# Optimization experiments

Hardware: AMD Instinct MI355X
Metric: run time of the kernel (lower is better)

## Reference

```python
import jax, jax.numpy as jnp
import numpy as np

N = 50000   # nodes
E = 400000  # edges
R = 35      # num_relations
B = 12      # num_bases
C = 128     # hidden_conv_dim (heads=1)
T = 4       # node types: load, gen, load_gen, ext
HL = 38     # hidden_lin_dim
OUT = 2


def setup_inputs() -> dict:
    key = jax.random.key(0)
    ks = jax.random.split(key, 24)
    s = 0.1  # param scale
    inp = {
        'x': jax.random.normal(ks[0], (N, 2), jnp.float32),
        'edge_index': jax.random.randint(ks[1], (2, E), 0, N, jnp.int32),
        'edge_type': jax.random.randint(ks[2], (E,), 0, R, jnp.int32),
        'edge_attr': jax.random.normal(ks[3], (E, 2), jnp.float32),
        'node_type': jax.random.randint(ks[4], (N,), 0, T, jnp.int32),
        'basis': jax.random.normal(ks[5], (B, 2, C), jnp.float32) * s,
        'att_rel': jax.random.normal(ks[6], (R, B), jnp.float32) * s,
        'q_att': jax.random.normal(ks[7], (C, 1), jnp.float32) * s,
        'k_att': jax.random.normal(ks[8], (C, 1), jnp.float32) * s,
        'e_att': jax.random.normal(ks[9], (C, 1), jnp.float32) * s,
        'lin_edge_W': jax.random.normal(ks[10], (2, C), jnp.float32) * s,
        'conv_bias': jax.random.normal(ks[11], (C,), jnp.float32) * s,
        'lin0_W': jax.random.normal(ks[12], (T, C, HL), jnp.float32) * s,
        'lin0_b': jax.random.normal(ks[13], (T, HL), jnp.float32) * s,
        'lin1_W': jax.random.normal(ks[14], (T, HL, HL), jnp.float32) * s,
        'lin1_b': jax.random.normal(ks[15], (T, HL), jnp.float32) * s,
        'lin2_W': jax.random.normal(ks[16], (T, HL, HL), jnp.float32) * s,
        'lin2_b': jax.random.normal(ks[17], (T, HL), jnp.float32) * s,
        'fin_W': jax.random.normal(ks[18], (T, HL, OUT), jnp.float32) * s,
        'fin_b': jax.random.normal(ks[19], (T, OUT), jnp.float32) * s,
    }
    return inp


def _segment_softmax(alpha, dst, n):
    # PyG softmax: max is detached, eps=1e-16 on the denominator
    amax = jax.lax.stop_gradient(jax.ops.segment_max(alpha, dst, num_segments=n))
    ex = jnp.exp(alpha - amax[dst])
    den = jax.ops.segment_sum(ex, dst, num_segments=n) + 1e-16
    return ex / den[dst]


def _per_type_linear(xv, W, b, t):
    # apply node-type-specific Linear: [N,d] x [T,d,h] -> pick row type
    y = jnp.einsum('nd,tdh->nth', xv, W)              # [N,T,h]
    y = jnp.take_along_axis(y, t[:, None, None], axis=1)[:, 0]
    return y + b[t]


def reference(x, edge_index, edge_type, edge_attr, node_type,
              basis, att_rel, q_att, k_att, e_att, lin_edge_W, conv_bias,
              lin0_W, lin0_b, lin1_W, lin1_b, lin2_W, lin2_b, fin_W, fin_b):
    n = x.shape[0]
    src, dst = edge_index[0], edge_index[1]
    # RGATConv with basis decomposition: per-relation weight [R, in=2, C]
    w = jnp.einsum('rb,bio->rio', att_rel, basis)
    w_e = w[edge_type]                                 # [E,2,C] edge gather
    out_i = jnp.einsum('ei,eic->ec', x[dst], w_e)      # [E,C]
    out_j = jnp.einsum('ei,eic->ec', x[src], w_e)      # [E,C]
    ke = (edge_attr @ lin_edge_W) @ e_att              # [E,1]
    alpha = out_i @ q_att + out_j @ k_att + ke         # additive self-attention
    alpha = jax.nn.leaky_relu(alpha, 0.2)
    alpha = _segment_softmax(alpha, dst, n)            # across-relation segment softmax
    msg = alpha * out_j                                # heads=1 -> [E,C]
    agg = jax.ops.segment_sum(msg, dst, num_segments=n) + conv_bias
    h = jax.nn.leaky_relu(agg, 0.2)                    # forward activation (dropout: eval)
    t = node_type
    h = _per_type_linear(jax.nn.relu(h), lin0_W, lin0_b, t)
    h = _per_type_linear(jax.nn.relu(h), lin1_W, lin1_b, t)
    h = _per_type_linear(jax.nn.relu(h), lin2_W, lin2_b, t)
    out = _per_type_linear(h, fin_W, fin_b, t)         # [N,2]
    # load nodes (type 0): second output passes through abs
    load_out = jnp.concatenate([out[:, :1], jnp.abs(out[:, 1:2])], axis=1)
    return jnp.where((t == 0)[:, None], load_out, out)
```

## Files before the change

### kernel.cpp

```cpp
#include <hip/hip_runtime.h>
#include <math.h>

#define N_NODES 50000
#define N_EDGES 400000
#define R_REL   35
#define B_BASES 12
#define C_DIM   128
#define HL_DIM  38
#define RI2     70
#define NP      50304
#define NB_HIST 196
#define NBUCK   786
#define EPB     2048
#define CAP     704

#define OFF_WT     0
#define OFF_WQ     8960
#define OFF_WK     9030
#define OFF_LE     9100
#define OFF_META   9104
#define OFF_HBLK   9120
#define OFF_PERM   10688
#define OFF_INV    60688
#define OFF_ECUR   110992
#define OFF_EREC   111780

#define ST    0
#define WT    4760
#define HH    0
#define Y0T   0
#define Y1T   3264
#define Y2T   0
#define W1S   8192
#define W2S   9720
#define W0F   13720
#define SM_DINV 18888
#define SM_FW   18952
#define SM_FB   19028
#define LDS_FLOATS 19030

__global__ __launch_bounds__(256) void k_init(const int* __restrict__ node_type,
                                              const float* __restrict__ basis,
                                              const float* __restrict__ att_rel,
                                              const float* __restrict__ q_att,
                                              const float* __restrict__ k_att,
                                              const float* __restrict__ e_att,
                                              const float* __restrict__ lin_edge_W,
                                              float* __restrict__ ws) {
    int b = blockIdx.x, tid = threadIdx.x;
    if (b < NB_HIST) {
        __shared__ int lh[4];
        if (tid < 4) lh[tid] = 0;
        __syncthreads();
        int i = b * 256 + tid;
        if (i < N_NODES) atomicAdd(&lh[node_type[i]], 1);
        __syncthreads();
        if (tid < 4) ((int*)(ws + OFF_HBLK))[b * 4 + tid] = lh[tid];
    } else if (b < NB_HIST + 35) {
        int idx = (b - NB_HIST) * 256 + tid;
        if (idx < RI2 * C_DIM) {
            int c  = idx & (C_DIM - 1);
            int ri = idx >> 7;
            int r = ri >> 1, ii = ri & 1;
            float acc = 0.f;
            #pragma unroll
            for (int bb = 0; bb < B_BASES; ++bb)
                acc += att_rel[r * B_BASES + bb] * basis[(bb * 2 + ii) * C_DIM + c];
            ws[OFF_WT + idx] = acc;
        }
    } else if (b == NB_HIST + 35) {
        for (int i = tid; i < NBUCK; i += 256) ((int*)(ws + OFF_ECUR))[i] = 0;
    } else {
        int lane = tid & 63, wv = tid >> 6;
        int u = (b - (NB_HIST + 36)) * 4 + wv;
        if (u < 2 * RI2) {
            int ri = (u < RI2) ? u : (u - RI2);
            int r = ri >> 1, ii = ri & 1;
            const float* av = att_rel + r * B_BASES;
            const float* bs = basis + ii * C_DIM;
            float w1 = 0.f, w2 = 0.f;
            #pragma unroll
            for (int bb = 0; bb < B_BASES; ++bb) {
                float a = av[bb];
                w1 += a * bs[bb * 2 * C_DIM + lane];
                w2 += a * bs[bb * 2 * C_DIM + 64 + lane];
            }
            const float* qk = (u < RI2) ? q_att : k_att;
            float s = w1 * qk[lane] + w2 * qk[64 + lane];
            #pragma unroll
            for (int off = 32; off; off >>= 1) s += __shfl_xor(s, off, 64);
            if (lane == 0) ws[((u < RI2) ? OFF_WQ : OFF_WK) + ri] = s;
        } else if (u < 2 * RI2 + 2) {
            int j = u - 2 * RI2;
            const float* er = lin_edge_W + j * C_DIM;
            float s = er[lane] * e_att[lane] + er[64 + lane] * e_att[64 + lane];
            #pragma unroll
            for (int off = 32; off; off >>= 1) s += __shfl_xor(s, off, 64);
            if (lane == 0) ws[OFF_LE + j] = s;
        }
    }
}

__global__ __launch_bounds__(256) void k_perm(const int* __restrict__ node_type,
                                              float* __restrict__ ws) {
    __shared__ int lh[NB_HIST * 4];
    __shared__ int pre[4], tot[4], basel[4];
    __shared__ int wcnt[4][4];
    int tid = threadIdx.x;
    int lane = tid & 63, wv = tid >> 6;
    const int* hblk = (const int*)(ws + OFF_HBLK);
    for (int i = tid; i < NB_HIST * 4; i += 256) lh[i] = hblk[i];
    __syncthreads();
    if (tid < 4) {
        int run = 0, mypre = 0;
        for (int bb = 0; bb < NB_HIST; ++bb) {
            if (bb == (int)blockIdx.x) mypre = run;
            run += lh[bb * 4 + tid];
        }
        pre[tid] = mypre;
        tot[tid] = run;
    }
    __syncthreads();
    if (tid == 0) {
        int t0 = tot[0], t1 = tot[1], t2 = tot[2];
        int b1 = ((t0 + 63) >> 6) << 6;
        int b2 = b1 + (((t1 + 63) >> 6) << 6);
        int b3 = b2 + (((t2 + 63) >> 6) << 6);
        basel[0] = 0; basel[1] = b1; basel[2] = b2; basel[3] = b3;
        if (blockIdx.x == 0) {
            int* meta = (int*)(ws + OFF_META);
            meta[0] = t0; meta[1] = t1; meta[2] = t2; meta[3] = tot[3];
            meta[4] = 0;  meta[5] = b1; meta[6] = b2; meta[7] = b3;
        }
    }
    __syncthreads();
    int n = blockIdx.x * 256 + tid;
    bool active = n < N_NODES;
    int ty = active ? node_type[n] : -1;
    int myrank = 0;
    #pragma unroll
    for (int t = 0; t < 4; ++t) {
        unsigned long long m = __ballot(ty == t);
        if (lane == 0) wcnt[wv][t] = __popcll(m);
        if (ty == t) myrank = __popcll(m & ((1ULL << lane) - 1ULL));
    }
    __syncthreads();
    if (active) {
        int prew = 0;
        for (int w2 = 0; w2 < wv; ++w2) prew += wcnt[w2][ty];
        int p = basel[ty] + pre[ty] + prew + myrank;
        ((int*)(ws + OFF_PERM))[n] = p;
        ((int*)(ws + OFF_INV))[p] = n;
    }
}

__global__ __launch_bounds__(256) void k_escatter(const float* __restrict__ x,
                                                  const int* __restrict__ edge_index,
                                                  const int* __restrict__ edge_type,
                                                  const float* __restrict__ edge_attr,
                                                  float* __restrict__ ws) {
    __shared__ int hist[NBUCK];
    __shared__ int sbase[NBUCK];
    __shared__ float swq[RI2], swk[RI2], sle[2];
    int tid = threadIdx.x;
    for (int i = tid; i < NBUCK; i += 256) hist[i] = 0;
    if (tid < RI2) { swq[tid] = ws[OFF_WQ + tid]; swk[tid] = ws[OFF_WK + tid]; }
    if (tid < 2) sle[tid] = ws[OFF_LE + tid];
    __syncthreads();

    const int* perm = (const int*)(ws + OFF_PERM);
    int base = blockIdx.x * EPB;
    int   rb[8], rm[8];
    float rex[8], rsx[8], rsy[8];
    #pragma unroll
    for (int k = 0; k < 8; ++k) {
        int e = base + k * 256 + tid;
        rb[k] = -1;
        if (e < N_EDGES) {
            int src = edge_index[e];
            int dst = edge_index[N_EDGES + e];
            int r   = edge_type[e];
            int p   = perm[dst];
            float2 ea = *(const float2*)(edge_attr + 2 * e);
            float2 xs = *(const float2*)(x + 2 * src);
            float2 xd = *(const float2*)(x + 2 * dst);
            float alpha = xd.x * swq[2 * r] + xd.y * swq[2 * r + 1]
                        + xs.x * swk[2 * r] + xs.y * swk[2 * r + 1]
                        + ea.x * sle[0]     + ea.y * sle[1];
            alpha = alpha > 0.f ? alpha : 0.2f * alpha;
            float ex = __expf(alpha);
            rb[k]  = p >> 6;
            rm[k]  = (r << 6) | (p & 63);
            rex[k] = ex;
            rsx[k] = ex * xs.x;
            rsy[k] = ex * xs.y;
            atomicAdd(&hist[rb[k]], 1);
        }
    }
    __syncthreads();
    int* gcur = (int*)(ws + OFF_ECUR);
    for (int i = tid; i < NBUCK; i += 256) {
        int c = hist[i];
        sbase[i] = (c > 0) ? atomicAdd(&gcur[i], c) : 0;
    }
    __syncthreads();
    float4* rec = (float4*)(ws + OFF_EREC);
    #pragma unroll
    for (int k = 0; k < 8; ++k) {
        if (rb[k] >= 0) {
            int slot = atomicAdd(&sbase[rb[k]], 1);
            rec[(size_t)rb[k] * CAP + slot] =
                make_float4(__int_as_float(rm[k]), rex[k], rsx[k], rsy[k]);
        }
    }
}

__global__ __launch_bounds__(256) void k_node(
        const float* __restrict__ ws, const float* __restrict__ conv_bias,
        const float* __restrict__ lin0_W, const float* __restrict__ lin0_b,
        const float* __restrict__ lin1_W, const float* __restrict__ lin1_b,
        const float* __restrict__ lin2_W, const float* __restrict__ lin2_b,
        const float* __restrict__ fin_W,  const float* __restrict__ fin_b,
        float* __restrict__ out) {
    __shared__ float L[LDS_FLOATS];
    int tid  = threadIdx.x;
    int lane = tid & 63;
    int wv   = tid >> 6;
    int p0   = blockIdx.x * 64;

    const int* meta = (const int*)(ws + OFF_META);
    int b1 = meta[5], b2 = meta[6], b3 = meta[7];
    int t  = (p0 >= b1) + (p0 >= b2) + (p0 >= b3);
    int bp = meta[4 + t];
    int cnt = meta[t];

    for (int i = tid; i < RI2 * 68; i += 256) L[ST + i] = 0.f;
    if (tid < 64) L[SM_DINV + tid] = 0.f;
    if (tid >= 64 && tid < 142) {
        int i = tid - 64;
        if (i < 76) L[SM_FW + i] = fin_W[t * 76 + i];
        else        L[SM_FB + i - 76] = fin_b[t * 2 + i - 76];
    }
    const float* wT_g = ws + OFF_WT;
    for (int i4 = tid; i4 < 2240; i4 += 256) {
        float4 v = ((const float4*)wT_g)[i4];
        *(float4*)&L[WT + i4 * 4] = v;
    }
    const float* W0g = lin0_W + t * C_DIM * HL_DIM;
    for (int i = tid; i < C_DIM * HL_DIM; i += 256) {
        int cc = i / 38, j = i - cc * 38;
        L[W0F + cc * 40 + j] = W0g[i];
    }
    __syncthreads();

    {
        int ecnt = ((const int*)(ws + OFF_ECUR))[blockIdx.x];
        const float4* rec = (const float4*)(ws + OFF_EREC) + (size_t)blockIdx.x * CAP;
        for (int i = tid; i < ecnt; i += 256) {
            float4 v = rec[i];
            int m = __float_as_int(v.x);
            int n = m & 63, r = m >> 6;
            atomicAdd(&L[ST + (2 * r) * 68 + n],     v.z);
            atomicAdd(&L[ST + (2 * r + 1) * 68 + n], v.w);
            atomicAdd(&L[SM_DINV + n],               v.y);
        }
    }
    __syncthreads();
    if (tid < 64) L[SM_DINV + tid] = 1.0f / (L[SM_DINV + tid] + 1e-16f);

    int ng = lane & 15, cg_ = lane >> 4;
    int c0 = wv * 32 + cg_ * 8;
    float acc[32];
    #pragma unroll
    for (int i = 0; i < 32; ++i) acc[i] = 0.f;
    #pragma unroll 5
    for (int kk = 0; kk < RI2; ++kk) {
        float4 a4 = *(const float4*)&L[ST + kk * 68 + ng * 4];
        float4 wa = *(const float4*)&L[WT + kk * 128 + c0];
        float4 wc = *(const float4*)&L[WT + kk * 128 + c0 + 4];
        float a_[4] = {a4.x, a4.y, a4.z, a4.w};
        float w_[8] = {wa.x, wa.y, wa.z, wa.w, wc.x, wc.y, wc.z, wc.w};
        #pragma unroll
        for (int ni = 0; ni < 4; ++ni)
            #pragma unroll
            for (int ci = 0; ci < 8; ++ci)
                acc[ni * 8 + ci] += a_[ni] * w_[ci];
    }
    __syncthreads();

    {
        float4 dv = *(const float4*)&L[SM_DINV + ng * 4];
        float d_[4] = {dv.x, dv.y, dv.z, dv.w};
        #pragma unroll
        for (int ci = 0; ci < 8; ++ci) {
            float cb = conv_bias[c0 + ci];
            float4 hv;
            float h0 = acc[0 * 8 + ci] * d_[0] + cb;
            float h1 = acc[1 * 8 + ci] * d_[1] + cb;
            float h2 = acc[2 * 8 + ci] * d_[2] + cb;
            float h3 = acc[3 * 8 + ci] * d_[3] + cb;
            hv.x = h0 > 0.f ? h0 : 0.f;
            hv.y = h1 > 0.f ? h1 : 0.f;
            hv.z = h2 > 0.f ? h2 : 0.f;
            hv.w = h3 > 0.f ? h3 : 0.f;
            *(float4*)&L[HH + (c0 + ci) * 64 + ng * 4] = hv;
        }
    }
    {
        const float* W1g = lin1_W + t * HL_DIM * HL_DIM;
        const float* W2g = lin2_W + t * HL_DIM * HL_DIM;
        for (int i = tid; i < HL_DIM * HL_DIM; i += 256) {
            int cc = i / 38, j = i - cc * 38;
            L[W1S + cc * 40 + j] = W1g[i];
            L[W2S + cc * 40 + j] = W2g[i];
        }
    }
    __syncthreads();

    int jg = lane >> 4;
    int j0 = wv * 16 + jg * 4;
    float acc2[16];
    #pragma unroll
    for (int i = 0; i < 16; ++i) acc2[i] = 0.f;
    if (wv < 3) {
        #pragma unroll 4
        for (int kk = 0; kk < C_DIM; ++kk) {
            float4 a4 = *(const float4*)&L[HH + kk * 64 + ng * 4];
            float4 w4 = *(const float4*)&L[W0F + kk * 40 + j0];
            float a_[4] = {a4.x, a4.y, a4.z, a4.w};
            float w_[4] = {w4.x, w4.y, w4.z, w4.w};
            #pragma unroll
            for (int ni = 0; ni < 4; ++ni)
                #pragma unroll
                for (int ji = 0; ji < 4; ++ji)
                    acc2[ni * 4 + ji] += a_[ni] * w_[ji];
        }
    }
    __syncthreads();

    if (wv < 3) {
        #pragma unroll
        for (int ji = 0; ji < 4; ++ji) {
            int j = j0 + ji;
            float b = (j < HL_DIM) ? lin0_b[t * HL_DIM + j] : 0.f;
            float4 yv;
            float y0 = acc2[0 * 4 + ji] + b;
            float y1 = acc2[1 * 4 + ji] + b;
            float y2 = acc2[2 * 4 + ji] + b;
            float y3 = acc2[3 * 4 + ji] + b;
            yv.x = y0 > 0.f ? y0 : 0.f;
            yv.y = y1 > 0.f ? y1 : 0.f;
            yv.z = y2 > 0.f ? y2 : 0.f;
            yv.w = y3 > 0.f ? y3 : 0.f;
            *(float4*)&L[Y0T + j * 68 + ng * 4] = yv;
        }
    }
    __syncthreads();

    if (wv < 3) {
        float acc3[16];
        #pragma unroll
        for (int i = 0; i < 16; ++i) acc3[i] = 0.f;
        #pragma unroll 2
        for (int kk = 0; kk < HL_DIM; ++kk) {
            float4 a4 = *(const float4*)&L[Y0T + kk * 68 + ng * 4];
            float4 w4 = *(const float4*)&L[W1S + kk * 40 + j0];
            float a_[4] = {a4.x, a4.y, a4.z, a4.w};
            float w_[4] = {w4.x, w4.y, w4.z, w4.w};
            #pragma unroll
            for (int ni = 0; ni < 4; ++ni)
                #pragma unroll
                for (int ji = 0; ji < 4; ++ji)
                    acc3[ni * 4 + ji] += a_[ni] * w_[ji];
        }
        #pragma unroll
        for (int ji = 0; ji < 4; ++ji) {
            int j = j0 + ji;
            float b = (j < HL_DIM) ? lin1_b[t * HL_DIM + j] : 0.f;
            float4 yv;
            float y0 = acc3[0 * 4 + ji] + b;
            float y1 = acc3[1 * 4 + ji] + b;
            float y2 = acc3[2 * 4 + ji] + b;
            float y3 = acc3[3 * 4 + ji] + b;
            yv.x = y0 > 0.f ? y0 : 0.f;
            yv.y = y1 > 0.f ? y1 : 0.f;
            yv.z = y2 > 0.f ? y2 : 0.f;
            yv.w = y3 > 0.f ? y3 : 0.f;
            *(float4*)&L[Y1T + j * 68 + ng * 4] = yv;
        }
    }
    __syncthreads();

    if (wv < 3) {
        float acc4[16];
        #pragma unroll
        for (int i = 0; i < 16; ++i) acc4[i] = 0.f;
        #pragma unroll 2
        for (int kk = 0; kk < HL_DIM; ++kk) {
            float4 a4 = *(const float4*)&L[Y1T + kk * 68 + ng * 4];
            float4 w4 = *(const float4*)&L[W2S + kk * 40 + j0];
            float a_[4] = {a4.x, a4.y, a4.z, a4.w};
            float w_[4] = {w4.x, w4.y, w4.z, w4.w};
            #pragma unroll
            for (int ni = 0; ni < 4; ++ni)
                #pragma unroll
                for (int ji = 0; ji < 4; ++ji)
                    acc4[ni * 4 + ji] += a_[ni] * w_[ji];
        }
        #pragma unroll
        for (int ji = 0; ji < 4; ++ji) {
            int j = j0 + ji;
            float b = (j < HL_DIM) ? lin2_b[t * HL_DIM + j] : 0.f;
            float4 yv;
            yv.x = acc4[0 * 4 + ji] + b;
            yv.y = acc4[1 * 4 + ji] + b;
            yv.z = acc4[2 * 4 + ji] + b;
            yv.w = acc4[3 * 4 + ji] + b;
            *(float4*)&L[Y2T + j * 68 + ng * 4] = yv;
        }
    }
    __syncthreads();

    if (tid < 64) {
        int p = p0 + tid;
        bool valid = (p - bp) < cnt;
        float o0 = L[SM_FB], o1 = L[SM_FB + 1];
        for (int jj = 0; jj < HL_DIM; ++jj) {
            float v = L[Y2T + jj * 68 + tid];
            float2 f = *(const float2*)&L[SM_FW + jj * 2];
            o0 += v * f.x;
            o1 += v * f.y;
        }
        if (t == 0) o1 = fabsf(o1);
        if (valid) {
            int orig = ((const int*)(ws + OFF_INV))[p];
            ((float2*)out)[orig] = make_float2(o0, o1);
        }
    }
}

extern "C" void kernel_launch(void* const* d_in, const int* in_sizes, int n_in,
                              void* d_out, int out_size, void* d_ws, size_t ws_size,
                              hipStream_t stream) {
    const float* x          = (const float*)d_in[0];
    const int*   edge_index = (const int*)  d_in[1];
    const int*   edge_type  = (const int*)  d_in[2];
    const float* edge_attr  = (const float*)d_in[3];
    const int*   node_type  = (const int*)  d_in[4];
    const float* basis      = (const float*)d_in[5];
    const float* att_rel    = (const float*)d_in[6];
    const float* q_att      = (const float*)d_in[7];
    const float* k_att      = (const float*)d_in[8];
    const float* e_att      = (const float*)d_in[9];
    const float* lin_edge_W = (const float*)d_in[10];
    const float* conv_bias  = (const float*)d_in[11];
    const float* lin0_W     = (const float*)d_in[12];
    const float* lin0_b     = (const float*)d_in[13];
    const float* lin1_W     = (const float*)d_in[14];
    const float* lin1_b     = (const float*)d_in[15];
    const float* lin2_W     = (const float*)d_in[16];
    const float* lin2_b     = (const float*)d_in[17];
    const float* fin_W      = (const float*)d_in[18];
    const float* fin_b      = (const float*)d_in[19];

    float* ws  = (float*)d_ws;
    float* out = (float*)d_out;

    k_init    <<<NB_HIST + 35 + 1 + 36, 256, 0, stream>>>(node_type, basis, att_rel,
                                                          q_att, k_att, e_att, lin_edge_W, ws);
    k_perm    <<<NB_HIST, 256, 0, stream>>>(node_type, ws);
    k_escatter<<<NB_HIST, 256, 0, stream>>>(x, edge_index, edge_type, edge_attr, ws);
    k_node    <<<NBUCK, 256, 0, stream>>>(ws, conv_bias,
                                          lin0_W, lin0_b, lin1_W, lin1_b,
                                          lin2_W, lin2_b, fin_W, fin_b, out);
}
```

Baseline: 172.9 us.

## Read node-MLP weights from padded global buffers instead of staging in LDS

k_init now repacks lin0/lin1/lin2 weights into padded (stride 40) global workspace buffers. k_node stops copying the relation weight table and MLP weights into shared memory and reads them directly from global/L2, which shrinks LDS from ~76KB to ~33KB per block and adds a launch bound of 4 blocks. The aim is to remove per-block staging traffic and raise occupancy, at the cost of broadcast-style global loads inside the inner GEMM loops and possible register pressure from the tighter launch bound.

```diff
diff --git a/kernel.cpp b/kernel.cpp
--- a/kernel.cpp
+++ b/kernel.cpp
@@ -24,20 +24,19 @@
 #define OFF_INV    60688
 #define OFF_ECUR   110992
 #define OFF_EREC   111780
+#define OFF_W0P    2325156
+#define OFF_W1P    2345636
+#define OFF_W2P    2351716
 
 #define ST    0
-#define WT    4760
 #define HH    0
 #define Y0T   0
 #define Y1T   3264
 #define Y2T   0
-#define W1S   8192
-#define W2S   9720
-#define W0F   13720
-#define SM_DINV 18888
-#define SM_FW   18952
-#define SM_FB   19028
-#define LDS_FLOATS 19030
+#define SM_DINV 8192
+#define SM_FW   8256
+#define SM_FB   8332
+#define LDS_FLOATS 8334
 
 __global__ __launch_bounds__(256) void k_init(const int* __restrict__ node_type,
                                               const float* __restrict__ basis,
@@ -46,6 +45,9 @@
                                               const float* __restrict__ k_att,
                                               const float* __restrict__ e_att,
                                               const float* __restrict__ lin_edge_W,
+                                              const float* __restrict__ lin0_W,
+                                              const float* __restrict__ lin1_W,
+                                              const float* __restrict__ lin2_W,
                                               float* __restrict__ ws) {
     int b = blockIdx.x, tid = threadIdx.x;
     if (b < NB_HIST) {
@@ -70,7 +72,7 @@
         }
     } else if (b == NB_HIST + 35) {
         for (int i = tid; i < NBUCK; i += 256) ((int*)(ws + OFF_ECUR))[i] = 0;
-    } else {
+    } else if (b < NB_HIST + 36 + 36) {
         int lane = tid & 63, wv = tid >> 6;
         int u = (b - (NB_HIST + 36)) * 4 + wv;
         if (u < 2 * RI2) {
@@ -97,6 +99,21 @@
             #pragma unroll
             for (int off = 32; off; off >>= 1) s += __shfl_xor(s, off, 64);
             if (lane == 0) ws[OFF_LE + j] = s;
+        }
+    } else {
+        int g = (b - (NB_HIST + 36 + 36)) * 256 + tid;
+        for (int idx = g; idx < 4 * C_DIM * HL_DIM; idx += 16 * 256) {
+            int tt = idx / (C_DIM * HL_DIM);
+            int rem = idx - tt * (C_DIM * HL_DIM);
+            int cc = rem / HL_DIM, j = rem - cc * HL_DIM;
+            ws[OFF_W0P + tt * (C_DIM * 40) + cc * 40 + j] = lin0_W[idx];
+        }
+        for (int idx = g; idx < 4 * HL_DIM * HL_DIM; idx += 16 * 256) {
+            int tt = idx / (HL_DIM * HL_DIM);
+            int rem = idx - tt * (HL_DIM * HL_DIM);
+            int cc = rem / HL_DIM, j = rem - cc * HL_DIM;
+            ws[OFF_W1P + tt * (HL_DIM * 40) + cc * 40 + j] = lin1_W[idx];
+            ws[OFF_W2P + tt * (HL_DIM * 40) + cc * 40 + j] = lin2_W[idx];
         }
     }
 }
@@ -215,13 +232,11 @@
     }
 }
 
-__global__ __launch_bounds__(256) void k_node(
+__global__ __launch_bounds__(256, 4) void k_node(
         const float* __restrict__ ws, const float* __restrict__ conv_bias,
-        const float* __restrict__ lin0_W, const float* __restrict__ lin0_b,
-        const float* __restrict__ lin1_W, const float* __restrict__ lin1_b,
-        const float* __restrict__ lin2_W, const float* __restrict__ lin2_b,
-        const float* __restrict__ fin_W,  const float* __restrict__ fin_b,
-        float* __restrict__ out) {
+        const float* __restrict__ lin0_b, const float* __restrict__ lin1_b,
+        const float* __restrict__ lin2_b, const float* __restrict__ fin_W,
+        const float* __restrict__ fin_b, float* __restrict__ out) {
     __shared__ float L[LDS_FLOATS];
     int tid  = threadIdx.x;
     int lane = tid & 63;
@@ -234,22 +249,13 @@
     int bp = meta[4 + t];
     int cnt = meta[t];
 
-    for (int i = tid; i < RI2 * 68; i += 256) L[ST + i] = 0.f;
+    for (int i4 = tid; i4 < (RI2 * 68) / 4; i4 += 256)
+        *(float4*)&L[ST + i4 * 4] = make_float4(0.f, 0.f, 0.f, 0.f);
     if (tid < 64) L[SM_DINV + tid] = 0.f;
     if (tid >= 64 && tid < 142) {
         int i = tid - 64;
         if (i < 76) L[SM_FW + i] = fin_W[t * 76 + i];
         else        L[SM_FB + i - 76] = fin_b[t * 2 + i - 76];
-    }
-    const float* wT_g = ws + OFF_WT;
-    for (int i4 = tid; i4 < 2240; i4 += 256) {
-        float4 v = ((const float4*)wT_g)[i4];
-        *(float4*)&L[WT + i4 * 4] = v;
-    }
-    const float* W0g = lin0_W + t * C_DIM * HL_DIM;
-    for (int i = tid; i < C_DIM * HL_DIM; i += 256) {
-        int cc = i / 38, j = i - cc * 38;
-        L[W0F + cc * 40 + j] = W0g[i];
     }
     __syncthreads();
 
@@ -270,14 +276,15 @@
 
     int ng = lane & 15, cg_ = lane >> 4;
     int c0 = wv * 32 + cg_ * 8;
+    const float* wTg = ws + OFF_WT;
     float acc[32];
     #pragma unroll
     for (int i = 0; i < 32; ++i) acc[i] = 0.f;
     #pragma unroll 5
     for (int kk = 0; kk < RI2; ++kk) {
         float4 a4 = *(const float4*)&L[ST + kk * 68 + ng * 4];
-        float4 wa = *(const float4*)&L[WT + kk * 128 + c0];
-        float4 wc = *(const float4*)&L[WT + kk * 128 + c0 + 4];
+        float4 wa = *(const float4*)&wTg[kk * 128 + c0];
+        float4 wc = *(const float4*)&wTg[kk * 128 + c0 + 4];
         float a_[4] = {a4.x, a4.y, a4.z, a4.w};
         float w_[8] = {wa.x, wa.y, wa.z, wa.w, wc.x, wc.y, wc.z, wc.w};
         #pragma unroll
@@ -306,19 +313,11 @@
             *(float4*)&L[HH + (c0 + ci) * 64 + ng * 4] = hv;
         }
     }
-    {
-        const float* W1g = lin1_W + t * HL_DIM * HL_DIM;
-        const float* W2g = lin2_W + t * HL_DIM * HL_DIM;
-        for (int i = tid; i < HL_DIM * HL_DIM; i += 256) {
-            int cc = i / 38, j = i - cc * 38;
-            L[W1S + cc * 40 + j] = W1g[i];
-            L[W2S + cc * 40 + j] = W2g[i];
-        }
-    }
     __syncthreads();
 
     int jg = lane >> 4;
     int j0 = wv * 16 + jg * 4;
+    const float* W0g = ws + OFF_W0P + t * (C_DIM * 40);
     float acc2[16];
     #pragma unroll
     for (int i = 0; i < 16; ++i) acc2[i] = 0.f;
@@ -326,7 +325,7 @@
         #pragma unroll 4
         for (int kk = 0; kk < C_DIM; ++kk) {
             float4 a4 = *(const float4*)&L[HH + kk * 64 + ng * 4];
-            float4 w4 = *(const float4*)&L[W0F + kk * 40 + j0];
+            float4 w4 = *(const float4*)&W0g[kk * 40 + j0];
             float a_[4] = {a4.x, a4.y, a4.z, a4.w};
             float w_[4] = {w4.x, w4.y, w4.z, w4.w};
             #pragma unroll
@@ -358,13 +357,14 @@
     __syncthreads();
 
     if (wv < 3) {
+        const float* W1g = ws + OFF_W1P + t * (HL_DIM * 40);
         float acc3[16];
         #pragma unroll
         for (int i = 0; i < 16; ++i) acc3[i] = 0.f;
         #pragma unroll 2
         for (int kk = 0; kk < HL_DIM; ++kk) {
             float4 a4 = *(const float4*)&L[Y0T + kk * 68 + ng * 4];
-            float4 w4 = *(const float4*)&L[W1S + kk * 40 + j0];
+            float4 w4 = *(const float4*)&W1g[kk * 40 + j0];
             float a_[4] = {a4.x, a4.y, a4.z, a4.w};
             float w_[4] = {w4.x, w4.y, w4.z, w4.w};
             #pragma unroll
@@ -392,13 +392,14 @@
     __syncthreads();
 
     if (wv < 3) {
+        const float* W2g = ws + OFF_W2P + t * (HL_DIM * 40);
         float acc4[16];
         #pragma unroll
         for (int i = 0; i < 16; ++i) acc4[i] = 0.f;
         #pragma unroll 2
         for (int kk = 0; kk < HL_DIM; ++kk) {
             float4 a4 = *(const float4*)&L[Y1T + kk * 68 + ng * 4];
-            float4 w4 = *(const float4*)&L[W2S + kk * 40 + j0];
+            float4 w4 = *(const float4*)&W2g[kk * 40 + j0];
             float a_[4] = {a4.x, a4.y, a4.z, a4.w};
             float w_[4] = {w4.x, w4.y, w4.z, w4.w};
             #pragma unroll
@@ -466,11 +467,11 @@
     float* ws  = (float*)d_ws;
     float* out = (float*)d_out;
 
-    k_init    <<<NB_HIST + 35 + 1 + 36, 256, 0, stream>>>(node_type, basis, att_rel,
-                                                          q_att, k_att, e_att, lin_edge_W, ws);
+    k_init    <<<NB_HIST + 35 + 1 + 36 + 16, 256, 0, stream>>>(node_type, basis, att_rel,
+                                                               q_att, k_att, e_att, lin_edge_W,
+                                                               lin0_W, lin1_W, lin2_W, ws);
     k_perm    <<<NB_HIST, 256, 0, stream>>>(node_type, ws);
     k_escatter<<<NB_HIST, 256, 0, stream>>>(x, edge_index, edge_type, edge_attr, ws);
     k_node    <<<NBUCK, 256, 0, stream>>>(ws, conv_bias,
-                                          lin0_W, lin0_b, lin1_W, lin1_b,
-                                          lin2_W, lin2_b, fin_W, fin_b, out);
+                                          lin0_b, lin1_b, lin2_b, fin_W, fin_b, out);
 }
```

New measurement: 168.6 us. 2.5% less time.
